# Performance work log

Measured on AMD Instinct MI355X. Metric: run time of the kernel, lower is better.

Reference implementation:

```python
import jax, jax.numpy as jnp
import numpy as np

NUM_CLASSES = 100
CLUSTERS_PER_CLASS = 64
LATENT_DIM = 128
BATCH = 32768


def setup_inputs() -> dict:
    key = jax.random.key(0)
    kx, kc, kl = jax.random.split(key, 3)
    x = jax.random.normal(kx, (BATCH, LATENT_DIM), dtype=jnp.float32)
    # nn.Parameter(torch.randn(C, Kc, D) * 0.1)
    centers = jax.random.normal(kc, (NUM_CLASSES, CLUSTERS_PER_CLASS, LATENT_DIM), dtype=jnp.float32) * 0.1
    labels = jax.random.randint(kl, (BATCH,), 0, NUM_CLASSES, dtype=jnp.int64)
    return {"x": x, "centers": centers, "labels": labels}


def reference(x, centers, labels):
    # [C, Kc, D] -> [K, D]
    all_centers = centers.reshape(-1, LATENT_DIM).astype(x.dtype)
    x2 = jnp.sum(x * x, axis=-1, keepdims=True)            # [B,1]
    c2 = jnp.sum(all_centers * all_centers, axis=-1)       # [K]
    sq = x2 + c2[None, :] - 2.0 * jnp.einsum('bd,kd->bk', x, all_centers)
    distances = jnp.sqrt(jnp.maximum(sq, 0.0))             # [B,K]
    closest_indices = jnp.argmin(distances, axis=1)        # [B]
    class_predictions = closest_indices // CLUSTERS_PER_CLASS
    cluster_assignments = closest_indices % CLUSTERS_PER_CLASS
    quantized_hard = all_centers[closest_indices]          # [B,D]
    min_distances = jnp.take_along_axis(distances, closest_indices[:, None], axis=1)[:, 0]
    # straight-through estimator (training path in the torch module)
    quantized = x + jax.lax.stop_gradient(quantized_hard - x)
    return quantized, cluster_assignments, min_distances, class_predictions
```

## Files before the change

### kernel.cpp

```cpp
#include <hip/hip_runtime.h>
#include <math.h>

#define BATCH  32768
#define D      128
#define K      6400
#define KC     64
#define ROWS_PER_BLOCK 64
#define CHUNK_C 128
#define HALVES 2
#define CHUNKS_PER_HALF 25

typedef _Float16 half8 __attribute__((ext_vector_type(8)));
typedef float    floatx4 __attribute__((ext_vector_type(4)));

typedef __attribute__((address_space(3))) unsigned       lds_uint;
typedef __attribute__((address_space(1))) const unsigned glb_uint;

__device__ __forceinline__ void async_lds16(const void* g, void* l) {
    __builtin_amdgcn_global_load_lds((glb_uint*)g, (lds_uint*)l, 16, 0, 0);
}

__global__ __launch_bounds__(256) void pack_kernel(const float* __restrict__ centers,
                                                   _Float16* __restrict__ wh,
                                                   float* __restrict__ c2n) {
    int tid = blockIdx.x * 256 + threadIdx.x;
    int ch = tid >> 11;
    int u  = (tid >> 7) & 15;
    int cw = tid & 127;
    int center = ch * CHUNK_C + cw;
    const float* src = centers + (size_t)center * D + u * 8;
    float4 a = *(const float4*)src;
    float4 b = *(const float4*)(src + 4);
    float f[8] = {a.x, a.y, a.z, a.w, b.x, b.y, b.z, b.w};
    half8 h;
#pragma unroll
    for (int j = 0; j < 8; ++j) h[j] = (_Float16)f[j];
    *(half8*)(wh + (size_t)tid * 8) = h;

    if (blockIdx.x < K / KC) {
        int c_local = threadIdx.x >> 2, part = threadIdx.x & 3;
        int c = blockIdx.x * 64 + c_local;
        const float4* p = (const float4*)(centers + (size_t)c * D + part * 32);
        float s = 0.f;
#pragma unroll
        for (int i = 0; i < 8; ++i) {
            float4 v = p[i];
            s = fmaf(v.x, v.x, s); s = fmaf(v.y, v.y, s);
            s = fmaf(v.z, v.z, s); s = fmaf(v.w, v.w, s);
        }
        s += __shfl_xor(s, 1, 64);
        s += __shfl_xor(s, 2, 64);
        if (part == 0) c2n[c] = -0.5f * s;
    }
}

__global__ __launch_bounds__(256, 4) void dist_kernel(
    const float* __restrict__ x, const float* __restrict__ centers,
    const _Float16* __restrict__ wh, const float* __restrict__ c2n,
    float* __restrict__ ws_sq, int* __restrict__ ws_ix) {
    __shared__ char lds[32768];

    const int t    = threadIdx.x;
    const int w    = t >> 6;
    const int L    = t & 63;
    const int quad = L >> 4;
    const int n16  = L & 15;
    const int rowhalf = w & 1;
    const int chalf   = w >> 1;
    const int half = blockIdx.y;
    const int gr0  = blockIdx.x * ROWS_PER_BLOCK;

    half8 Ah[2][4];
#pragma unroll
    for (int rt = 0; rt < 2; ++rt) {
        int r = gr0 + rowhalf * 32 + rt * 16 + n16;
        const float* xr = x + (size_t)r * D + quad * 8;
#pragma unroll
        for (int ks = 0; ks < 4; ++ks) {
            float4 a = *(const float4*)(xr + ks * 32);
            float4 b = *(const float4*)(xr + ks * 32 + 4);
            float f[8] = {a.x, a.y, a.z, a.w, b.x, b.y, b.z, b.w};
            half8 h;
#pragma unroll
            for (int j = 0; j < 8; ++j) h[j] = (_Float16)f[j];
            Ah[rt][ks] = h;
        }
    }

    float b1[8], b2[8];
    int   j1_[8], j2_[8];
#pragma unroll
    for (int k = 0; k < 8; ++k) { b1[k] = -3.4e38f; b2[k] = -3.4e38f; j1_[k] = 0; j2_[k] = 0; }

    const char* gh = (const char*)wh + (size_t)half * CHUNKS_PER_HALF * 32768;

    for (int ch = 0; ch < CHUNKS_PER_HALF; ++ch) {
        __syncthreads();
#pragma unroll
        for (int i = 0; i < 8; ++i) {
            int seg = w + i * 4;
            async_lds16(gh + seg * 1024 + L * 16, lds + seg * 1024);
        }
        const int kbase = (half * CHUNKS_PER_HALF + ch) * CHUNK_C + chalf * 64;
        float c2v[4];
#pragma unroll
        for (int ct = 0; ct < 4; ++ct) c2v[ct] = c2n[kbase + ct * 16 + n16];
        __syncthreads();
        gh += 32768;

        floatx4 acc[2][4];
#pragma unroll
        for (int rt = 0; rt < 2; ++rt)
#pragma unroll
            for (int ct = 0; ct < 4; ++ct)
                acc[rt][ct] = (floatx4){c2v[ct], c2v[ct], c2v[ct], c2v[ct]};

#pragma unroll
        for (int ks = 0; ks < 4; ++ks) {
            const half8* pb = (const half8*)lds + (ks * 4 + quad) * 128 + chalf * 64 + n16;
#pragma unroll
            for (int ct = 0; ct < 4; ++ct) {
                half8 Bf = pb[ct * 16];
                acc[0][ct] = __builtin_amdgcn_mfma_f32_16x16x32_f16(Ah[0][ks], Bf, acc[0][ct], 0, 0, 0);
                acc[1][ct] = __builtin_amdgcn_mfma_f32_16x16x32_f16(Ah[1][ks], Bf, acc[1][ct], 0, 0, 0);
            }
        }

        int i0 = kbase + n16;
#pragma unroll
        for (int rt = 0; rt < 2; ++rt)
#pragma unroll
            for (int reg = 0; reg < 4; ++reg) {
                float s0 = acc[rt][0][reg], s1 = acc[rt][1][reg];
                float s2 = acc[rt][2][reg], s3 = acc[rt][3][reg];
                bool g01 = s1 > s0, g23 = s3 > s2;
                float m01 = g01 ? s1 : s0;  int x01 = g01 ? i0 + 16 : i0;
                float m23 = g23 ? s3 : s2;  int x23 = g23 ? i0 + 48 : i0 + 32;
                bool gq = m23 > m01;
                float q  = gq ? m23 : m01;  int qi = gq ? x23 : x01;
                int k = rt * 4 + reg;
                bool bet1 = q > b1[k];
                bool bet2 = q > b2[k];
                float nb2 = bet1 ? b1[k] : (bet2 ? q : b2[k]);
                int   nj2 = bet1 ? j1_[k] : (bet2 ? qi : j2_[k]);
                b1[k]  = bet1 ? q : b1[k];
                j1_[k] = bet1 ? qi : j1_[k];
                b2[k]  = nb2;
                j2_[k] = nj2;
            }
    }

    __syncthreads();
    int* candL = (int*)lds;

#pragma unroll
    for (int k = 0; k < 8; ++k) {
        float v1 = b1[k], v2 = b2[k];
        int   p1 = j1_[k], p2 = j2_[k];
#pragma unroll
        for (int m = 1; m < 8; m <<= 1) {
            float o1 = __shfl_xor(v1, m, 64), o2 = __shfl_xor(v2, m, 64);
            int   q1 = __shfl_xor(p1, m, 64), q2 = __shfl_xor(p2, m, 64);
            bool firstMine = (v1 > o1) || (v1 == o1 && p1 < q1);
            float nv1 = firstMine ? v1 : o1;  int np1 = firstMine ? p1 : q1;
            float cb  = firstMine ? o1 : v1;  int cpi = firstMine ? q1 : p1;
            float ob  = firstMine ? v2 : o2;  int obi = firstMine ? p2 : q2;
            bool secOwn = (ob > cb) || (ob == cb && obi < cpi);
            v1 = nv1; p1 = np1;
            v2 = secOwn ? ob : cb;  p2 = secOwn ? obi : cpi;
        }
        if ((n16 & 7) == 0) {
            int rloc = rowhalf * 32 + (k >> 2) * 16 + quad * 4 + (k & 3);
            int g = chalf * 2 + (n16 >> 3);
            candL[rloc * 8 + g * 2 + 0] = p1;
            candL[rloc * 8 + g * 2 + 1] = p2;
        }
    }
    __syncthreads();

    {
        int r = t >> 2, p = t & 3;
        int ixa = candL[r * 8 + p * 2 + 0];
        int ixb = candL[r * 8 + p * 2 + 1];
        const float4* xr4 = (const float4*)(x + (size_t)(gr0 + r) * D);
        const float4* ca4 = (const float4*)(centers + (size_t)ixa * D);
        const float4* cb4 = (const float4*)(centers + (size_t)ixb * D);
        float dota = 0.f, dotb = 0.f, x2s = 0.f, c2a = 0.f, c2b = 0.f;
#pragma unroll
        for (int d4 = 0; d4 < 32; ++d4) {
            float4 xv = xr4[d4], av = ca4[d4], bv = cb4[d4];
            dota = fmaf(xv.x, av.x, dota); dota = fmaf(xv.y, av.y, dota);
            dota = fmaf(xv.z, av.z, dota); dota = fmaf(xv.w, av.w, dota);
            dotb = fmaf(xv.x, bv.x, dotb); dotb = fmaf(xv.y, bv.y, dotb);
            dotb = fmaf(xv.z, bv.z, dotb); dotb = fmaf(xv.w, bv.w, dotb);
            x2s = fmaf(xv.x, xv.x, x2s); x2s = fmaf(xv.y, xv.y, x2s);
            x2s = fmaf(xv.z, xv.z, x2s); x2s = fmaf(xv.w, xv.w, x2s);
            c2a = fmaf(av.x, av.x, c2a); c2a = fmaf(av.y, av.y, c2a);
            c2a = fmaf(av.z, av.z, c2a); c2a = fmaf(av.w, av.w, c2a);
            c2b = fmaf(bv.x, bv.x, c2b); c2b = fmaf(bv.y, bv.y, c2b);
            c2b = fmaf(bv.z, bv.z, c2b); c2b = fmaf(bv.w, bv.w, c2b);
        }
        float sqa = x2s + c2a - 2.f * dota;
        float sqb = x2s + c2b - 2.f * dotb;
        bool aw = (sqa < sqb) || (sqa == sqb && ixa < ixb);
        float sq = aw ? sqa : sqb;
        int   ix = aw ? ixa : ixb;
#pragma unroll
        for (int m = 1; m < 4; m <<= 1) {
            float osq = __shfl_xor(sq, m, 64);
            int   oix = __shfl_xor(ix, m, 64);
            if (osq < sq || (osq == sq && oix < ix)) { sq = osq; ix = oix; }
        }
        if (p == 0) {
            ws_sq[(size_t)half * BATCH + gr0 + r] = sq;
            ws_ix[(size_t)half * BATCH + gr0 + r] = ix;
        }
    }
}

__global__ __launch_bounds__(256) void final_kernel(
    const float* __restrict__ x, const float* __restrict__ centers,
    const float* __restrict__ ws_sq, const int* __restrict__ ws_ix,
    float* __restrict__ out) {
    int g = blockIdx.x * 256 + threadIdx.x;
    int row = g >> 5, d4 = g & 31;

    float sqa = ws_sq[row],         sqb = ws_sq[BATCH + row];
    int   ixa = ws_ix[row],         ixb = ws_ix[BATCH + row];
    bool aw = (sqa <= sqb);
    float sq = aw ? sqa : sqb;
    int   ix = aw ? ixa : ixb;

    float* out_clu = out + (size_t)BATCH * D;
    float* out_md  = out_clu + BATCH;
    float* out_cls = out_md + BATCH;
    if (d4 == 0) {
        out_md[row]  = sqrtf(fmaxf(sq, 0.f));
        out_clu[row] = (float)(ix & (KC - 1));
        out_cls[row] = (float)(ix >> 6);
    }

    float4 cv = ((const float4*)centers)[(size_t)ix * 32 + d4];
    float4 xv = ((const float4*)x)[(size_t)row * 32 + d4];
    float4 o;
    o.x = xv.x + (cv.x - xv.x);
    o.y = xv.y + (cv.y - xv.y);
    o.z = xv.z + (cv.z - xv.z);
    o.w = xv.w + (cv.w - xv.w);
    ((float4*)out)[(size_t)row * 32 + d4] = o;
}

extern "C" void kernel_launch(void* const* d_in, const int* in_sizes, int n_in,
                              void* d_out, int out_size, void* d_ws, size_t ws_size,
                              hipStream_t stream) {
    const float* x       = (const float*)d_in[0];
    const float* centers = (const float*)d_in[1];
    float* out = (float*)d_out;

    _Float16* wh    = (_Float16*)d_ws;
    float*    c2n   = (float*)(wh + (size_t)K * D);
    float*    ws_sq = c2n + K;
    int*      ws_ix = (int*)(ws_sq + HALVES * BATCH);

    pack_kernel<<<(K * 16) / 256, 256, 0, stream>>>(centers, wh, c2n);
    dim3 grid(BATCH / ROWS_PER_BLOCK, HALVES);
    dist_kernel<<<grid, 256, 0, stream>>>(x, centers, wh, c2n, ws_sq, ws_ix);
    final_kernel<<<(BATCH * 32) / 256, 256, 0, stream>>>(x, centers, ws_sq, ws_ix, out);
}
```

Baseline: 204.3 us.

## Double-buffer center chunks in LDS and widen dist blocks to 128 rows

The distance kernel now prefetches the next 32KB half-precision center chunk into a second LDS buffer while MFMAs run on the current one. This replaces the two-barrier load-then-compute loop with a single barrier per chunk. Blocks grow to 512 threads covering 128 rows, so each staged center chunk is reused by twice as many rows, halving LDS fill traffic per row. LDS per block doubles to 64KB, which may cut resident blocks per CU and shifts occupancy.

Result: faster. 197.1 us (-3.5%).

```diff
diff --git a/kernel.cpp b/kernel.cpp
--- a/kernel.cpp
+++ b/kernel.cpp
@@ -5,7 +5,7 @@
 #define D      128
 #define K      6400
 #define KC     64
-#define ROWS_PER_BLOCK 64
+#define ROWS_PER_BLOCK 128
 #define CHUNK_C 128
 #define HALVES 2
 #define CHUNKS_PER_HALF 25
@@ -54,26 +54,26 @@
     }
 }
 
-__global__ __launch_bounds__(256, 4) void dist_kernel(
+__global__ __launch_bounds__(512, 4) void dist_kernel(
     const float* __restrict__ x, const float* __restrict__ centers,
     const _Float16* __restrict__ wh, const float* __restrict__ c2n,
     float* __restrict__ ws_sq, int* __restrict__ ws_ix) {
-    __shared__ char lds[32768];
+    __shared__ char lds[65536];
 
     const int t    = threadIdx.x;
     const int w    = t >> 6;
     const int L    = t & 63;
     const int quad = L >> 4;
     const int n16  = L & 15;
-    const int rowhalf = w & 1;
-    const int chalf   = w >> 1;
+    const int rq      = w >> 1;
+    const int chalf   = w & 1;
     const int half = blockIdx.y;
     const int gr0  = blockIdx.x * ROWS_PER_BLOCK;
 
     half8 Ah[2][4];
 #pragma unroll
     for (int rt = 0; rt < 2; ++rt) {
-        int r = gr0 + rowhalf * 32 + rt * 16 + n16;
+        int r = gr0 + rq * 32 + rt * 16 + n16;
         const float* xr = x + (size_t)r * D + quad * 8;
 #pragma unroll
         for (int ks = 0; ks < 4; ++ks) {
@@ -94,19 +94,29 @@
 
     const char* gh = (const char*)wh + (size_t)half * CHUNKS_PER_HALF * 32768;
 
-    for (int ch = 0; ch < CHUNKS_PER_HALF; ++ch) {
-        __syncthreads();
-#pragma unroll
-        for (int i = 0; i < 8; ++i) {
-            int seg = w + i * 4;
-            async_lds16(gh + seg * 1024 + L * 16, lds + seg * 1024);
-        }
-        const int kbase = (half * CHUNKS_PER_HALF + ch) * CHUNK_C + chalf * 64;
+#pragma unroll
+    for (int i = 0; i < 4; ++i) {
+        int seg = w + i * 8;
+        async_lds16(gh + seg * 1024 + L * 16, lds + seg * 1024);
+    }
+    __syncthreads();
+
+    for (int ci = 0; ci < CHUNKS_PER_HALF; ++ci) {
+        const char* cur = lds + (ci & 1) * 32768;
+        if (ci + 1 < CHUNKS_PER_HALF) {
+            const char* gn = gh + (ci + 1) * 32768;
+            char* nxt = lds + ((ci + 1) & 1) * 32768;
+#pragma unroll
+            for (int i = 0; i < 4; ++i) {
+                int seg = w + i * 8;
+                async_lds16(gn + seg * 1024 + L * 16, nxt + seg * 1024);
+            }
+        }
+
+        const int kbase = (half * CHUNKS_PER_HALF + ci) * CHUNK_C + chalf * 64;
         float c2v[4];
 #pragma unroll
         for (int ct = 0; ct < 4; ++ct) c2v[ct] = c2n[kbase + ct * 16 + n16];
-        __syncthreads();
-        gh += 32768;
 
         floatx4 acc[2][4];
 #pragma unroll
@@ -117,7 +127,7 @@
 
 #pragma unroll
         for (int ks = 0; ks < 4; ++ks) {
-            const half8* pb = (const half8*)lds + (ks * 4 + quad) * 128 + chalf * 64 + n16;
+            const half8* pb = (const half8*)cur + (ks * 4 + quad) * 128 + chalf * 64 + n16;
 #pragma unroll
             for (int ct = 0; ct < 4; ++ct) {
                 half8 Bf = pb[ct * 16];
@@ -137,20 +147,21 @@
                 float m01 = g01 ? s1 : s0;  int x01 = g01 ? i0 + 16 : i0;
                 float m23 = g23 ? s3 : s2;  int x23 = g23 ? i0 + 48 : i0 + 32;
                 bool gq = m23 > m01;
-                float q  = gq ? m23 : m01;  int qi = gq ? x23 : x01;
+                float v  = gq ? m23 : m01;  int vi = gq ? x23 : x01;
                 int k = rt * 4 + reg;
-                bool bet1 = q > b1[k];
-                bool bet2 = q > b2[k];
-                float nb2 = bet1 ? b1[k] : (bet2 ? q : b2[k]);
-                int   nj2 = bet1 ? j1_[k] : (bet2 ? qi : j2_[k]);
-                b1[k]  = bet1 ? q : b1[k];
-                j1_[k] = bet1 ? qi : j1_[k];
+                bool bet1 = v > b1[k];
+                bool bet2 = v > b2[k];
+                float nb2 = bet1 ? b1[k] : (bet2 ? v : b2[k]);
+                int   nj2 = bet1 ? j1_[k] : (bet2 ? vi : j2_[k]);
+                b1[k]  = bet1 ? v : b1[k];
+                j1_[k] = bet1 ? vi : j1_[k];
                 b2[k]  = nb2;
                 j2_[k] = nj2;
             }
-    }
-
-    __syncthreads();
+
+        __syncthreads();
+    }
+
     int* candL = (int*)lds;
 
 #pragma unroll
@@ -170,7 +181,7 @@
             v2 = secOwn ? ob : cb;  p2 = secOwn ? obi : cpi;
         }
         if ((n16 & 7) == 0) {
-            int rloc = rowhalf * 32 + (k >> 2) * 16 + quad * 4 + (k & 3);
+            int rloc = rq * 32 + (k >> 2) * 16 + quad * 4 + (k & 3);
             int g = chalf * 2 + (n16 >> 3);
             candL[rloc * 8 + g * 2 + 0] = p1;
             candL[rloc * 8 + g * 2 + 1] = p2;
@@ -264,6 +275,6 @@
 
     pack_kernel<<<(K * 16) / 256, 256, 0, stream>>>(centers, wh, c2n);
     dim3 grid(BATCH / ROWS_PER_BLOCK, HALVES);
-    dist_kernel<<<grid, 256, 0, stream>>>(x, centers, wh, c2n, ws_sq, ws_ix);
+    dist_kernel<<<grid, 512, 0, stream>>>(x, centers, wh, c2n, ws_sq, ws_ix);
     final_kernel<<<(BATCH * 32) / 256, 256, 0, stream>>>(x, centers, ws_sq, ws_ix, out);
 }
```
